# Performance work log

Hardware: AMD Instinct MI355X
Metric: run time of the kernel (lower is better)

Reference implementation:

```python
import jax, jax.numpy as jnp
import numpy as np
from jax import lax

THRESHOLD = 1.0  # threshold_potential from __init__
STRIDE = (1, 1)
PADDING = 'SAME'


def setup_inputs() -> dict:
    key = jax.random.key(0)
    k1, k2, k3 = jax.random.split(key, 3)
    input_to_layer = jax.random.normal(k1, (1, 512, 512, 16), dtype=jnp.float32)
    weights = jax.random.normal(k2, (3, 3, 16, 64), dtype=jnp.float32)
    old_potentials = jax.random.normal(k3, (1, 512, 512, 64), dtype=jnp.float32)
    return {
        'input_to_layer': input_to_layer,
        'weights': weights,
        'old_potentials': old_potentials,
    }


def reference(input_to_layer, weights, old_potentials):
    # conv2d NHWC x HWIO -> NHWC, SAME padding, stride 1 (as tf.nn.conv2d)
    out_conv = lax.conv_general_dilated(
        input_to_layer, weights,
        window_strides=STRIDE, padding=PADDING,
        dimension_numbers=('NHWC', 'HWIO', 'NHWC'))
    # accumulate membrane potential, fused threshold -> spike + reset
    new_potentials = out_conv + old_potentials
    spiked = new_potentials >= THRESHOLD
    curr_spikes = spiked.astype(new_potentials.dtype)
    new_potentials = jnp.where(spiked, 0.0, new_potentials)
    # original returns spikes; new_potentials is the updated state
    return curr_spikes, new_potentials
```

## Files before the change

kernel.cpp:

```cpp
#include <hip/hip_runtime.h>


#define H 512
#define W 512
#define CI 16
#define CO 64
#define PW 514
#define PAD_PX (PW * PW)
#define W3_OFF_U16 0
#define IN_OFF_U16 32768
#define NTILES 8
#define PF 3

typedef float v4f __attribute__((ext_vector_type(4)));
typedef float f32x4 __attribute__((ext_vector_type(4)));
typedef short short8 __attribute__((ext_vector_type(8)));
typedef unsigned int uint4v __attribute__((ext_vector_type(4)));

__device__ __forceinline__ unsigned int pack2bf(float f0, float f1) {
    unsigned u0 = __builtin_bit_cast(unsigned, f0);
    unsigned u1 = __builtin_bit_cast(unsigned, f1);
    u0 = (u0 + 0x7FFFu + ((u0 >> 16) & 1u)) >> 16;
    u1 = (u1 + 0x7FFFu + ((u1 >> 16) & 1u)) >> 16;
    return u0 | (u1 << 16);
}

__global__ void snn_setup(const float* __restrict__ in,
                          const float* __restrict__ w,
                          unsigned short* __restrict__ ws)
{
    const int tid = threadIdx.x;
    if (blockIdx.x == gridDim.x - 1) {
        uint4v* wf = (uint4v*)(ws + W3_OFF_U16);
        #pragma unroll
        for (int i = 0; i < 5; ++i) {
            const int f    = i * 256 + tid;
            const int ks5  = f >> 8;
            const int rem  = f & 255;
            const int nt   = rem >> 6;
            const int lane = rem & 63;
            const int r    = lane & 15;
            const int quad = lane >> 4;
            const int k0   = (ks5 < 4) ? (ks5 * 32 + quad * 8)
                                       : (128 + (quad & 1) * 8);
            const int co   = nt * 16 + r;
            uint4v v;
            #pragma unroll
            for (int m = 0; m < 4; ++m)
                v[m] = pack2bf(w[(k0 + 2 * m) * CO + co],
                               w[(k0 + 2 * m + 1) * CO + co]);
            wf[f] = v;
        }
        return;
    }
    const int p = blockIdx.x * 256 + tid;
    if (p >= PAD_PX) return;
    const int py = p / PW, px = p - py * PW;
    uint4v pk0 = (uint4v)0u, pk1 = (uint4v)0u;
    if (py >= 1 && py <= H && px >= 1 && px <= W) {
        const v4f* q = (const v4f*)(in + ((py - 1) * W + (px - 1)) * CI);
        v4f a = q[0], b = q[1], c = q[2], d = q[3];
        pk0 = (uint4v){pack2bf(a.x, a.y), pack2bf(a.z, a.w),
                       pack2bf(b.x, b.y), pack2bf(b.z, b.w)};
        pk1 = (uint4v){pack2bf(c.x, c.y), pack2bf(c.z, c.w),
                       pack2bf(d.x, d.y), pack2bf(d.z, d.w)};
    }
    uint4v* dst = (uint4v*)(ws + IN_OFF_U16 + p * CI);
    dst[0] = pk0;
    dst[1] = pk1;
}

__global__ __launch_bounds__(256, 2)
void snn_conv_mfma(const unsigned short* __restrict__ ws,
                   const float* __restrict__ oldp,
                   float* __restrict__ out_spk,
                   float* __restrict__ out_pot)
{
    const unsigned short* pin = ws + IN_OFF_U16;

    const int tid  = threadIdx.x;
    const int bx   = blockIdx.x & 31;
    const int g    = blockIdx.x >> 5;
    const int lane = tid & 63;
    const int wv   = tid >> 6;
    const int r    = lane & 15;
    const int quad = lane >> 4;
    const int half = quad & 1;
    const int tsel = quad >> 1;

    const int gx  = bx * 16 + r;
    const int gyB = g * (4 * NTILES) + wv;

    short8 bf[5][4];
    #pragma unroll
    for (int ks5 = 0; ks5 < 5; ++ks5)
        #pragma unroll
        for (int nt = 0; nt < 4; ++nt)
            bf[ks5][nt] = *(const short8*)&ws[(ks5 * 256 + nt * 64 + lane) * 8];

    short8 af[NTILES][5];
    f32x4  oldv[NTILES][4];

    auto issue = [&](int t) {
        const int gy = gyB + t * 4;
        const int eb = (gy * W + gx) * CO + quad * 4;
        #pragma unroll
        for (int nt = 0; nt < 4; ++nt)
            oldv[t][nt] = *(const f32x4*)(oldp + eb + nt * 16);
        #pragma unroll
        for (int ks5 = 0; ks5 < 4; ++ks5) {
            const int t8 = 2 * ks5 + tsel;
            const int dy = t8 / 3, dx = t8 % 3;
            af[t][ks5] = *(const short8*)
                &pin[((gy + dy) * PW + (gx + dx)) * CI + half * 8];
        }
        const int p4 = (quad < 2) ? ((gy + 2) * PW + (gx + 2)) : gx;
        af[t][4] = *(const short8*)&pin[p4 * CI + half * 8];
    };

    issue(0);
    issue(1);
    issue(2);

    #pragma unroll
    for (int t = 0; t < NTILES; ++t) {
        f32x4 acc[4] = {};
        #pragma unroll
        for (int ks5 = 0; ks5 < 5; ++ks5)
            #pragma unroll
            for (int nt = 0; nt < 4; ++nt)
                acc[nt] = __builtin_amdgcn_mfma_f32_16x16x32_bf16(
                    bf[ks5][nt], af[t][ks5], acc[nt], 0, 0, 0);

        const int gy = gyB + t * 4;
        const int eb = (gy * W + gx) * CO + quad * 4;
        #pragma unroll
        for (int nt = 0; nt < 4; ++nt) {
            const int idx = eb + nt * 16;
            f32x4 np = acc[nt] + oldv[t][nt];
            f32x4 spk, pot;
            #pragma unroll
            for (int j = 0; j < 4; ++j) {
                const bool s = np[j] >= 1.0f;
                spk[j] = s ? 1.0f : 0.0f;
                pot[j] = s ? 0.0f : np[j];
            }
            *(f32x4*)(out_spk + idx) = spk;
            *(f32x4*)(out_pot + idx) = pot;
        }

        if (t + PF < NTILES) issue(t + PF);
    }
}

extern "C" void kernel_launch(void* const* d_in, const int* in_sizes, int n_in,
                              void* d_out, int out_size, void* d_ws, size_t ws_size,
                              hipStream_t stream) {
    const float* in   = (const float*)d_in[0];
    const float* w    = (const float*)d_in[1];
    const float* oldp = (const float*)d_in[2];
    float* out_spk = (float*)d_out;
    float* out_pot = out_spk + (size_t)H * W * CO;
    unsigned short* ws = (unsigned short*)d_ws;

    const int setup_grid = (PAD_PX + 255) / 256 + 1;
    snn_setup<<<setup_grid, 256, 0, stream>>>(in, w, ws);

    const int grid = 32 * 16;
    snn_conv_mfma<<<grid, 256, 0, stream>>>(ws, oldp, out_spk, out_pot);
}
```

Before: 231.9 us.

## Stage conv inputs and old potentials in LDS via async global-to-LDS loads

Replaces the register-prefetched multi-tile loop with small 4x32-pixel blocks. Each block uses global_load_lds to stage the halo input rows and its old-potential tile into shared memory, then builds MFMA fragments from LDS. The grid grows from 512 to 2048 blocks and launch bounds move to 3 blocks per SIMD, trading the software pipelining inside each block for more parallelism across blocks and for reuse of the input halo. Each block now waits on a single __syncthreads, and the global-to-LDS loads must be correctly laid out for the MFMA reads.

```diff
diff --git a/kernel.cpp b/kernel.cpp
--- a/kernel.cpp
+++ b/kernel.cpp
@@ -9,8 +9,8 @@
 #define PAD_PX (PW * PW)
 #define W3_OFF_U16 0
 #define IN_OFF_U16 32768
-#define NTILES 8
-#define PF 3
+#define TXP 32
+#define TYP 4
 
 typedef float v4f __attribute__((ext_vector_type(4)));
 typedef float f32x4 __attribute__((ext_vector_type(4)));
@@ -23,6 +23,12 @@
     u0 = (u0 + 0x7FFFu + ((u0 >> 16) & 1u)) >> 16;
     u1 = (u1 + 0x7FFFu + ((u1 >> 16) & 1u)) >> 16;
     return u0 | (u1 << 16);
+}
+
+__device__ __forceinline__ void gload_lds16(void* lds, const void* g) {
+    __builtin_amdgcn_global_load_lds(
+        (const __attribute__((address_space(1))) unsigned int*)g,
+        (__attribute__((address_space(3))) unsigned int*)lds, 16, 0, 0);
 }
 
 __global__ void snn_setup(const float* __restrict__ in,
@@ -39,11 +45,11 @@
             const int rem  = f & 255;
             const int nt   = rem >> 6;
             const int lane = rem & 63;
-            const int r    = lane & 15;
+            const int rr   = lane & 15;
             const int quad = lane >> 4;
             const int k0   = (ks5 < 4) ? (ks5 * 32 + quad * 8)
                                        : (128 + (quad & 1) * 8);
-            const int co   = nt * 16 + r;
+            const int co   = nt * 16 + rr;
             uint4v v;
             #pragma unroll
             for (int m = 0; m < 4; ++m)
@@ -70,17 +76,20 @@
     dst[1] = pk1;
 }
 
-__global__ __launch_bounds__(256, 2)
+__global__ __launch_bounds__(256, 3)
 void snn_conv_mfma(const unsigned short* __restrict__ ws,
                    const float* __restrict__ oldp,
                    float* __restrict__ out_spk,
                    float* __restrict__ out_pot)
 {
+    __shared__ float s_old[TYP * TXP * CO];
+    __shared__ unsigned short s_i[6 * 64 * CI];
+
     const unsigned short* pin = ws + IN_OFF_U16;
 
     const int tid  = threadIdx.x;
-    const int bx   = blockIdx.x & 31;
-    const int g    = blockIdx.x >> 5;
+    const int bx   = blockIdx.x & 15;
+    const int by   = blockIdx.x >> 4;
     const int lane = tid & 63;
     const int wv   = tid >> 6;
     const int r    = lane & 15;
@@ -88,8 +97,29 @@
     const int half = quad & 1;
     const int tsel = quad >> 1;
 
-    const int gx  = bx * 16 + r;
-    const int gyB = g * (4 * NTILES) + wv;
+    const int gy0 = by * TYP;
+    const int gx0 = bx * TXP;
+
+    {
+        const char* src = (const char*)(oldp + ((gy0 + wv) * W + gx0) * CO)
+                          + lane * 16;
+        char* dst = (char*)s_old + wv * 8192;
+        #pragma unroll
+        for (int c = 0; c < 8; ++c)
+            gload_lds16(dst + c * 1024, src + c * 1024);
+    }
+    {
+        const int xs = gx0 - 16;
+        #pragma unroll
+        for (int k = 0; k < 3; ++k) {
+            const int c   = wv * 3 + k;
+            const int row = c >> 1, hf = c & 1;
+            const char* src = (const char*)(pin + ((gy0 + row) * PW + xs) * CI)
+                              + hf * 1024 + lane * 16;
+            char* dst = (char*)s_i + row * 2048 + hf * 1024;
+            gload_lds16(dst, src);
+        }
+    }
 
     short8 bf[5][4];
     #pragma unroll
@@ -98,46 +128,40 @@
         for (int nt = 0; nt < 4; ++nt)
             bf[ks5][nt] = *(const short8*)&ws[(ks5 * 256 + nt * 64 + lane) * 8];
 
-    short8 af[NTILES][5];
-    f32x4  oldv[NTILES][4];
+    __syncthreads();
 
-    auto issue = [&](int t) {
-        const int gy = gyB + t * 4;
-        const int eb = (gy * W + gx) * CO + quad * 4;
+    f32x4 acc[2][4] = {};
+    const short8 zero8 = {0, 0, 0, 0, 0, 0, 0, 0};
+    #pragma unroll
+    for (int ks5 = 0; ks5 < 5; ++ks5) {
+        const int t8 = (ks5 == 4) ? 8 : (2 * ks5 + tsel);
+        const int dy = t8 / 3, dx = t8 % 3;
+        short8 af[2];
         #pragma unroll
-        for (int nt = 0; nt < 4; ++nt)
-            oldv[t][nt] = *(const f32x4*)(oldp + eb + nt * 16);
+        for (int mt = 0; mt < 2; ++mt) {
+            const int px = mt * 16 + r + dx + 16;
+            short8 a = *(const short8*)&s_i[((wv + dy) * 64 + px) * CI + half * 8];
+            if (ks5 == 4) a = (quad >= 2) ? zero8 : a;
+            af[mt] = a;
+        }
         #pragma unroll
-        for (int ks5 = 0; ks5 < 4; ++ks5) {
-            const int t8 = 2 * ks5 + tsel;
-            const int dy = t8 / 3, dx = t8 % 3;
-            af[t][ks5] = *(const short8*)
-                &pin[((gy + dy) * PW + (gx + dx)) * CI + half * 8];
-        }
-        const int p4 = (quad < 2) ? ((gy + 2) * PW + (gx + 2)) : gx;
-        af[t][4] = *(const short8*)&pin[p4 * CI + half * 8];
-    };
-
-    issue(0);
-    issue(1);
-    issue(2);
+        for (int mt = 0; mt < 2; ++mt)
+            #pragma unroll
+            for (int nt = 0; nt < 4; ++nt)
+                acc[mt][nt] = __builtin_amdgcn_mfma_f32_16x16x32_bf16(
+                    bf[ks5][nt], af[mt], acc[mt][nt], 0, 0, 0);
+    }
 
     #pragma unroll
-    for (int t = 0; t < NTILES; ++t) {
-        f32x4 acc[4] = {};
-        #pragma unroll
-        for (int ks5 = 0; ks5 < 5; ++ks5)
-            #pragma unroll
-            for (int nt = 0; nt < 4; ++nt)
-                acc[nt] = __builtin_amdgcn_mfma_f32_16x16x32_bf16(
-                    bf[ks5][nt], af[t][ks5], acc[nt], 0, 0, 0);
-
-        const int gy = gyB + t * 4;
-        const int eb = (gy * W + gx) * CO + quad * 4;
+    for (int mt = 0; mt < 2; ++mt) {
+        const int gxo = gx0 + mt * 16 + r;
+        const int eb  = ((gy0 + wv) * W + gxo) * CO + quad * 4;
         #pragma unroll
         for (int nt = 0; nt < 4; ++nt) {
+            const f32x4 ov = *(const f32x4*)
+                &s_old[(wv * TXP + mt * 16 + r) * CO + nt * 16 + quad * 4];
             const int idx = eb + nt * 16;
-            f32x4 np = acc[nt] + oldv[t][nt];
+            f32x4 np = acc[mt][nt] + ov;
             f32x4 spk, pot;
             #pragma unroll
             for (int j = 0; j < 4; ++j) {
@@ -148,8 +172,6 @@
             *(f32x4*)(out_spk + idx) = spk;
             *(f32x4*)(out_pot + idx) = pot;
         }
-
-        if (t + PF < NTILES) issue(t + PF);
     }
 }
 
@@ -166,6 +188,6 @@
     const int setup_grid = (PAD_PX + 255) / 256 + 1;
     snn_setup<<<setup_grid, 256, 0, stream>>>(in, w, ws);
 
-    const int grid = 32 * 16;
+    const int grid = (W / TXP) * (H / TYP);
     snn_conv_mfma<<<grid, 256, 0, stream>>>(ws, oldp, out_spk, out_pot);
 }
```

Result: faster. 214.1 us (-7.7%).
